# Kernel optimization log

Measured on AMD Instinct MI355X. Metric: run time of the kernel, lower is better.

## Reference

```python
import jax, jax.numpy as jnp
import numpy as np

OUT_DIM = 1024


def setup_inputs() -> dict:
    key = jax.random.key(0)
    k1, k2, k3, k4 = jax.random.split(key, 4)
    B, N, D = 4, 2048, 1024
    s = 1.0 / np.sqrt(D)
    return {
        "x": jax.random.normal(k1, (B, N, D), dtype=jnp.float32),
        "W_query": jax.random.normal(k2, (D, OUT_DIM), dtype=jnp.float32) * s,
        "W_key": jax.random.normal(k3, (D, OUT_DIM), dtype=jnp.float32) * s,
        "W_value": jax.random.normal(k4, (D, OUT_DIM), dtype=jnp.float32) * s,
    }


def reference(x, W_query, W_key, W_value):
    # x: [B, N, D_in]; W_*: [D_in, D_out] (torch Linear weight transposed)
    q = jnp.einsum("bnd,de->bne", x, W_query)
    k = jnp.einsum("bnd,de->bne", x, W_key)
    v = jnp.einsum("bnd,de->bne", x, W_value)
    sqrt_d = jnp.sqrt(jnp.asarray(OUT_DIM, dtype=jnp.float32))
    scores = jnp.einsum("bie,bje->bij", q, k) / sqrt_d  # [B, N, N]
    # NOTE: original uses softmax over dim=1 (query axis), not the usual dim=2
    attn = jax.nn.softmax(scores, axis=1)
    # dropout with train=False is identity (eval-mode reference)
    # out = attn^T @ v  ->  out[b, j] = sum_i attn[b, i, j] * v[b, i]
    return jnp.einsum("bij,bie->bje", attn, v)
```

## Files before the change

### kernel.cpp

```cpp
#include <hip/hip_runtime.h>
#include <math.h>


typedef __bf16 bf16x8 __attribute__((ext_vector_type(8)));
typedef float f32x4 __attribute__((ext_vector_type(4)));

static __device__ __forceinline__ unsigned short f2bf(float f) {
    unsigned u = __float_as_uint(f);
    u += 0x7fff + ((u >> 16) & 1);
    return (unsigned short)(u >> 16);
}

#define GLDS16(gptr, lptr)                                                            \
    __builtin_amdgcn_global_load_lds(                                                 \
        (const __attribute__((address_space(1))) void*)(gptr),                        \
        (__attribute__((address_space(3))) void*)(lptr), 16, 0, 0)

#define BARSYNC  __builtin_amdgcn_s_barrier()
#define WAITLGKM do { asm volatile("s_waitcnt lgkmcnt(0)" ::: "memory");    \
                      __builtin_amdgcn_sched_barrier(0); } while (0)

__device__ __forceinline__ void gemm256_core(
    const unsigned short* __restrict__ Ab,
    const unsigned short* __restrict__ Bb,
    const long ld, unsigned short* lds, f32x4 acc[8][4])
{
    const int tid  = threadIdx.x;
    const int w    = tid >> 6;
    const int lane = tid & 63;

    const int r  = lane >> 3;
    const int s  = lane & 7;
    const int cg = (s ^ r) * 8;

    const int fr    = lane & 15;
    const int quad  = lane >> 4;
    const int sw    = fr & 7;
    const int arow0 = (w >> 2) * 128;
    const int brow0 = (w & 3) * 64;

#define STG_A(t, mh, buf) do {                                              \
    const int rb_ = (w >> 2) * 128 + (mh) * 64 + (w & 3) * 16;              \
    const unsigned short* g_ = Ab + (long)(rb_ + r) * ld + (long)(t) * 64 + cg; \
    unsigned short* d_ = lds + (buf) * 16384 + rb_ * 64;                    \
    GLDS16(g_, d_); GLDS16(g_ + 8 * ld, d_ + 512); } while (0)
#define STG_B(t, nh, buf) do {                                              \
    const int rb_ = (w >> 1) * 64 + (nh) * 32 + (w & 1) * 16;               \
    const unsigned short* g_ = Bb + (long)(rb_ + r) * ld + (long)(t) * 64 + cg; \
    unsigned short* d_ = lds + 32768 + (buf) * 16384 + rb_ * 64;            \
    GLDS16(g_, d_); GLDS16(g_ + 8 * ld, d_ + 512); } while (0)

    bf16x8 af[4][2], bfA[2][2], bfB[2][2];
#define LOADA(buf, mh) do {                                                 \
    _Pragma("unroll") for (int ks_ = 0; ks_ < 2; ks_++)                     \
    _Pragma("unroll") for (int i_ = 0; i_ < 4; i_++)                        \
        af[i_][ks_] = *(const bf16x8*)&lds[(buf) * 16384 +                  \
            (arow0 + (mh) * 64 + i_ * 16 + fr) * 64 +                       \
            ((ks_ * 4 + quad) ^ sw) * 8]; } while (0)
#define LOADB(BF, buf, nh) do {                                             \
    _Pragma("unroll") for (int ks_ = 0; ks_ < 2; ks_++)                     \
    _Pragma("unroll") for (int j_ = 0; j_ < 2; j_++)                        \
        BF[j_][ks_] = *(const bf16x8*)&lds[32768 + (buf) * 16384 +          \
            (brow0 + (nh) * 32 + j_ * 16 + fr) * 64 +                       \
            ((ks_ * 4 + quad) ^ sw) * 8]; } while (0)

#define MFMA16(mh, nh, BF) do {                                             \
    __builtin_amdgcn_s_setprio(1);                                          \
    _Pragma("unroll") for (int ks_ = 0; ks_ < 2; ks_++)                     \
    _Pragma("unroll") for (int i_ = 0; i_ < 4; i_++)                        \
    _Pragma("unroll") for (int j_ = 0; j_ < 2; j_++)                        \
        acc[(mh) * 4 + i_][(nh) * 2 + j_] =                                 \
            __builtin_amdgcn_mfma_f32_16x16x32_bf16(                        \
                af[i_][ks_], BF[j_][ks_],                                   \
                acc[(mh) * 4 + i_][(nh) * 2 + j_], 0, 0, 0);                \
    __builtin_amdgcn_s_setprio(0); } while (0)

#pragma unroll
    for (int i = 0; i < 8; i++)
#pragma unroll
        for (int j = 0; j < 4; j++) acc[i][j] = f32x4{0.f, 0.f, 0.f, 0.f};

    STG_A(0, 0, 0); STG_A(0, 1, 0); STG_B(0, 0, 0); STG_B(0, 1, 0);
    STG_A(1, 0, 1); STG_B(1, 1, 1);
    asm volatile("s_waitcnt vmcnt(4)" ::: "memory");
    BARSYNC;

#pragma unroll 1
    for (int i = 0; i < 8; ++i) {
        const int t1 = 2 * i + 1;
        const int t2 = (2 * i + 2) & 15;
        const int t3 = (2 * i + 3) & 15;
        LOADA(0, 0); LOADB(bfA, 0, 0); STG_B(t1, 0, 1);
        BARSYNC; WAITLGKM; MFMA16(0, 0, bfA); BARSYNC;
        LOADB(bfB, 0, 1); STG_A(t1, 1, 1);
        BARSYNC; WAITLGKM; MFMA16(0, 1, bfB); BARSYNC;
        LOADA(0, 1); STG_A(t2, 0, 0);
        BARSYNC; WAITLGKM; MFMA16(1, 1, bfB); BARSYNC;
        STG_B(t2, 1, 0);
        BARSYNC; MFMA16(1, 0, bfA);
        asm volatile("s_waitcnt vmcnt(4)" ::: "memory"); BARSYNC;
        LOADA(1, 0); LOADB(bfA, 1, 0); STG_A(t2, 1, 0);
        BARSYNC; WAITLGKM; MFMA16(0, 0, bfA); BARSYNC;
        LOADB(bfB, 1, 1); STG_B(t2, 0, 0);
        BARSYNC; WAITLGKM; MFMA16(0, 1, bfB); BARSYNC;
        LOADA(1, 1); STG_A(t3, 0, 1);
        BARSYNC; WAITLGKM; MFMA16(1, 1, bfB); BARSYNC;
        STG_B(t3, 1, 1);
        BARSYNC; MFMA16(1, 0, bfA);
        asm volatile("s_waitcnt vmcnt(4)" ::: "memory"); BARSYNC;
    }
    asm volatile("s_waitcnt vmcnt(0)" ::: "memory");

#undef STG_A
#undef STG_B
#undef LOADA
#undef LOADB
#undef MFMA16
}

__device__ __forceinline__ void pv256_core(
    const unsigned short* __restrict__ Ab,
    const unsigned short* __restrict__ Bb,
    unsigned short* lds, f32x4 acc[8][2])
{
    const int tid  = threadIdx.x;
    const int w    = tid >> 6;
    const int lane = tid & 63;

    const int r  = lane >> 3;
    const int s  = lane & 7;
    const int cg = (s ^ r) * 8;

    const int fr    = lane & 15;
    const int quad  = lane >> 4;
    const int sw    = fr & 7;
    const int arow0 = (w >> 2) * 128;
    const int brow0 = (w & 3) * 32;

#define STG_PA(t, mh, buf) do {                                             \
    const int rb_ = (w >> 2) * 128 + (mh) * 64 + (w & 3) * 16;              \
    const unsigned short* g_ = Ab + (long)(rb_ + r) * 2048 + (long)(t) * 64 + cg; \
    unsigned short* d_ = lds + (buf) * 16384 + rb_ * 64;                    \
    GLDS16(g_, d_); GLDS16(g_ + 8 * 2048, d_ + 512); } while (0)
#define STG_PB(t, nh, buf) do {                                             \
    const int rb_ = (w & 3) * 32 + (nh) * 16 + (w >> 2) * 8;                \
    const unsigned short* g_ = Bb + (long)(rb_ + r) * 8192 + (long)(t) * 64 + cg; \
    unsigned short* d_ = lds + 32768 + (buf) * 8192 + rb_ * 64;             \
    GLDS16(g_, d_); } while (0)

    bf16x8 af[4][2], bfA[2], bfB[2];
#define LOADPA(buf, mh) do {                                                \
    _Pragma("unroll") for (int ks_ = 0; ks_ < 2; ks_++)                     \
    _Pragma("unroll") for (int i_ = 0; i_ < 4; i_++)                        \
        af[i_][ks_] = *(const bf16x8*)&lds[(buf) * 16384 +                  \
            (arow0 + (mh) * 64 + i_ * 16 + fr) * 64 +                       \
            ((ks_ * 4 + quad) ^ sw) * 8]; } while (0)
#define LOADPB(BF, buf, nh) do {                                            \
    _Pragma("unroll") for (int ks_ = 0; ks_ < 2; ks_++)                     \
        BF[ks_] = *(const bf16x8*)&lds[32768 + (buf) * 8192 +               \
            (brow0 + (nh) * 16 + fr) * 64 +                                 \
            ((ks_ * 4 + quad) ^ sw) * 8]; } while (0)

#define MFMA8(mh, nh, BF) do {                                              \
    __builtin_amdgcn_s_setprio(1);                                          \
    _Pragma("unroll") for (int ks_ = 0; ks_ < 2; ks_++)                     \
    _Pragma("unroll") for (int i_ = 0; i_ < 4; i_++)                        \
        acc[(mh) * 4 + i_][nh] = __builtin_amdgcn_mfma_f32_16x16x32_bf16(   \
            af[i_][ks_], BF[ks_], acc[(mh) * 4 + i_][nh], 0, 0, 0);         \
    __builtin_amdgcn_s_setprio(0); } while (0)

#pragma unroll
    for (int i = 0; i < 8; i++)
#pragma unroll
        for (int j = 0; j < 2; j++) acc[i][j] = f32x4{0.f, 0.f, 0.f, 0.f};

    STG_PA(0, 0, 0); STG_PA(0, 1, 0); STG_PB(0, 0, 0); STG_PB(0, 1, 0);
    STG_PA(1, 0, 1); STG_PB(1, 1, 1);
    asm volatile("s_waitcnt vmcnt(3)" ::: "memory");
    BARSYNC;

#pragma unroll 1
    for (int i = 0; i < 16; ++i) {
        const int t1 = 2 * i + 1;
        const int t2 = (2 * i + 2) & 31;
        const int t3 = (2 * i + 3) & 31;
        LOADPA(0, 0); LOADPB(bfA, 0, 0); STG_PB(t1, 0, 1);
        BARSYNC; WAITLGKM; MFMA8(0, 0, bfA); BARSYNC;
        LOADPB(bfB, 0, 1); STG_PA(t1, 1, 1);
        BARSYNC; WAITLGKM; MFMA8(0, 1, bfB); BARSYNC;
        LOADPA(0, 1); STG_PA(t2, 0, 0);
        BARSYNC; WAITLGKM; MFMA8(1, 1, bfB); BARSYNC;
        STG_PB(t2, 1, 0);
        BARSYNC; MFMA8(1, 0, bfA);
        asm volatile("s_waitcnt vmcnt(3)" ::: "memory"); BARSYNC;
        LOADPA(1, 0); LOADPB(bfA, 1, 0); STG_PA(t2, 1, 0);
        BARSYNC; WAITLGKM; MFMA8(0, 0, bfA); BARSYNC;
        LOADPB(bfB, 1, 1); STG_PB(t2, 0, 0);
        BARSYNC; WAITLGKM; MFMA8(0, 1, bfB); BARSYNC;
        LOADPA(1, 1); STG_PA(t3, 0, 1);
        BARSYNC; WAITLGKM; MFMA8(1, 1, bfB); BARSYNC;
        STG_PB(t3, 1, 1);
        BARSYNC; MFMA8(1, 0, bfA);
        asm volatile("s_waitcnt vmcnt(3)" ::: "memory"); BARSYNC;
    }
    asm volatile("s_waitcnt vmcnt(0)" ::: "memory");

#undef STG_PA
#undef STG_PB
#undef LOADPA
#undef LOADPB
#undef MFMA8
}

__global__ __launch_bounds__(512, 2) void gemm_qkv256(
    const unsigned short* __restrict__ A, const unsigned short* __restrict__ B,
    unsigned short* __restrict__ QK, unsigned short* __restrict__ Vt)
{
    __shared__ unsigned short lds[65536];
    const int orig = blockIdx.x;
    const int xcd  = orig & 7;
    const int pos  = orig >> 3;
    const long gm0 = (long)(xcd * 4 + (pos & 3)) * 256;
    const long gn0 = (long)(pos >> 2) * 256;

    f32x4 acc[8][4];
    gemm256_core(A + gm0 * 1024, B + gn0 * 1024, 1024, lds, acc);

    const int tid = threadIdx.x;
    const int w = tid >> 6, lane = tid & 63;
    const int fr = lane & 15, quad = lane >> 4;
    const int wm = (w >> 2) * 128, wn = (w & 3) * 64;

    if (gn0 < 2048) {
#pragma unroll
        for (int mi = 0; mi < 8; mi++) {
            const long rb = gm0 + wm + (mi >> 2) * 64 + (mi & 3) * 16 + quad * 4;
#pragma unroll
            for (int n = 0; n < 4; n++) {
                const long cb = gn0 + wn + n * 16 + fr;
#pragma unroll
                for (int rr = 0; rr < 4; rr++)
                    QK[(rb + rr) * 2048L + cb] = f2bf(acc[mi][n][rr]);
            }
        }
    } else {
#pragma unroll
        for (int mi = 0; mi < 8; mi++) {
            const long rb = gm0 + wm + (mi >> 2) * 64 + (mi & 3) * 16 + quad * 4;
#pragma unroll
            for (int n = 0; n < 4; n++) {
                const long ce = gn0 - 2048 + wn + n * 16 + fr;
                ushort4 o;
                o.x = f2bf(acc[mi][n][0]);
                o.y = f2bf(acc[mi][n][1]);
                o.z = f2bf(acc[mi][n][2]);
                o.w = f2bf(acc[mi][n][3]);
                *(ushort4*)&Vt[ce * 8192L + rb] = o;
            }
        }
    }
}

__global__ __launch_bounds__(512, 2) void gemm_scores256(
    const unsigned short* __restrict__ QKb, unsigned short* __restrict__ P,
    float* __restrict__ l)
{
    __shared__ unsigned short lds[65536];
    const int orig = blockIdx.x;
    const int xcd  = orig & 7;
    const int pos  = orig >> 3;
    const int bz   = xcd >> 1;
    const long gm0 = (long)((xcd & 1) * 4 + (pos >> 3)) * 256;
    const long gn0 = (long)(pos & 7) * 256;

    const unsigned short* Ab = QKb + (long)bz * 2048 * 2048 + 1024 + gm0 * 2048;
    const unsigned short* Bb = QKb + (long)bz * 2048 * 2048 + gn0 * 2048;

    f32x4 acc[8][4];
    gemm256_core(Ab, Bb, 2048, lds, acc);

    const int tid = threadIdx.x;
    const int w = tid >> 6, lane = tid & 63;
    const int fr = lane & 15, quad = lane >> 4;
    const int wm = (w >> 2) * 128, wn = (w & 3) * 64;

    unsigned short* Pb = P + (long)bz * 2048 * 2048;
    float* lb = l + (long)bz * 2048;
    const float scale = 1.0f / 32.0f;
#pragma unroll
    for (int mi = 0; mi < 8; mi++) {
        const long rb = gm0 + wm + (mi >> 2) * 64 + (mi & 3) * 16 + quad * 4;
        float rs[4] = {0.f, 0.f, 0.f, 0.f};
#pragma unroll
        for (int n = 0; n < 4; n++) {
            const long cb = gn0 + wn + n * 16 + fr;
#pragma unroll
            for (int rr = 0; rr < 4; rr++) {
                float e = __expf(acc[mi][n][rr] * scale);
                rs[rr] += e;
                Pb[(rb + rr) * 2048L + cb] = f2bf(e);
            }
        }
#pragma unroll
        for (int rr = 0; rr < 4; rr++) {
#pragma unroll
            for (int m = 8; m > 0; m >>= 1) rs[rr] += __shfl_xor(rs[rr], m, 16);
        }
        if (fr == 0) {
#pragma unroll
            for (int rr = 0; rr < 4; rr++)
                atomicAdd(&lb[rb + rr], rs[rr]);
        }
    }
}

__global__ __launch_bounds__(512, 2) void gemm_pv256(
    const unsigned short* __restrict__ P, const unsigned short* __restrict__ Vt,
    const float* __restrict__ l, float* __restrict__ out)
{
    __shared__ unsigned short lds[49152];
    const int orig = blockIdx.x;
    const int xcd  = orig & 7;
    const int pos  = orig >> 3;
    const int bz   = xcd >> 1;
    const long gm0 = (long)((xcd & 1) * 4 + (pos >> 3)) * 256;
    const long gn0 = (long)(pos & 7) * 128;

    const unsigned short* Ab = P + (long)bz * 2048 * 2048 + gm0 * 2048;
    const unsigned short* Bb = Vt + gn0 * 8192 + (long)bz * 2048;

    f32x4 acc[8][2];
    pv256_core(Ab, Bb, lds, acc);

    const int tid = threadIdx.x;
    const int w = tid >> 6, lane = tid & 63;
    const int fr = lane & 15, quad = lane >> 4;
    const int wm = (w >> 2) * 128, wn = (w & 3) * 32;

    float* Ob = out + (long)bz * 2048 * 1024;
    const float* lb = l + (long)bz * 2048;
#pragma unroll
    for (int mi = 0; mi < 8; mi++) {
        const long rb = gm0 + wm + (mi >> 2) * 64 + (mi & 3) * 16 + quad * 4;
        float inv[4];
#pragma unroll
        for (int rr = 0; rr < 4; rr++) inv[rr] = 1.0f / lb[rb + rr];
#pragma unroll
        for (int nj = 0; nj < 2; nj++) {
            const long cb = gn0 + wn + nj * 16 + fr;
#pragma unroll
            for (int rr = 0; rr < 4; rr++)
                Ob[(rb + rr) * 1024L + cb] = acc[mi][nj][rr] * inv[rr];
        }
    }
}

__global__ __launch_bounds__(256) void prep(
    const float* __restrict__ x,
    const float* __restrict__ Wq, const float* __restrict__ Wk,
    const float* __restrict__ Wv,
    unsigned short* __restrict__ xb, unsigned short* __restrict__ Wqkvt,
    float* __restrict__ l)
{
    __shared__ float t[32][33];
    const int b = blockIdx.x;
    const int tid = threadIdx.x;
    if (b < 8192) {
        int i = b * 256 + tid;
        float4 v = ((const float4*)x)[i];
        ushort4 o;
        o.x = f2bf(v.x); o.y = f2bf(v.y); o.z = f2bf(v.z); o.w = f2bf(v.w);
        ((ushort4*)xb)[i] = o;
        return;
    }
    if (b == 8192 + 3072) {
        float4 z = {0.f, 0.f, 0.f, 0.f};
#pragma unroll
        for (int i = 0; i < 8; i++)
            ((float4*)l)[tid * 8 + i] = z;
        return;
    }
    int tix = b - 8192;
    const int w = tix >> 10;
    tix &= 1023;
    const float* W = (w == 0) ? Wq : (w == 1) ? Wk : Wv;
    unsigned short* Wt = Wqkvt + (long)w * 1024 * 1024;
    const int bx = (tix & 31) * 32;
    const int by = (tix >> 5) * 32;
    const int tx = tid & 31;
    const int ty = (tid >> 5) * 4;
#pragma unroll
    for (int j = 0; j < 4; j++)
        t[ty + j][tx] = W[(long)(by + ty + j) * 1024 + bx + tx];
    __syncthreads();
#pragma unroll
    for (int j = 0; j < 4; j++)
        Wt[(long)(bx + ty + j) * 1024 + by + tx] = f2bf(t[tx][ty + j]);
}

extern "C" void kernel_launch(void* const* d_in, const int* in_sizes, int n_in,
                              void* d_out, int out_size, void* d_ws,
                              size_t ws_size, hipStream_t stream)
{
    const float* x  = (const float*)d_in[0];
    const float* Wq = (const float*)d_in[1];
    const float* Wk = (const float*)d_in[2];
    const float* Wv = (const float*)d_in[3];
    float* out = (float*)d_out;

    const long M1 = 1024 * 1024;
    unsigned short* u     = (unsigned short*)d_ws;
    unsigned short* xb    = u;
    unsigned short* Wqkvt = u + 8 * M1;
    unsigned short* QKb   = Wqkvt + 3 * M1;
    unsigned short* Vtb   = QKb + 16 * M1;
    unsigned short* Pb    = Vtb + 8 * M1;
    float* l              = (float*)(Pb + 16 * M1);

    prep<<<dim3(8192 + 3072 + 1), dim3(256), 0, stream>>>(x, Wq, Wk, Wv, xb, Wqkvt, l);

    gemm_qkv256<<<dim3(384), dim3(512), 0, stream>>>(xb, Wqkvt, QKb, Vtb);

    gemm_scores256<<<dim3(256), dim3(512), 0, stream>>>(QKb, Pb, l);

    gemm_pv256<<<dim3(256), dim3(512), 0, stream>>>(Pb, Vtb, l, out);
}
```

Measured before the change: 227.4 us.

## Split QKV GEMM into QK kernel and separate 128x256-tile V kernel

```diff
diff --git a/kernel.cpp b/kernel.cpp
--- a/kernel.cpp
+++ b/kernel.cpp
@@ -118,6 +118,104 @@
 #undef MFMA16
 }
 
+__device__ __forceinline__ void gemm_v128_core(
+    const unsigned short* __restrict__ Ab,
+    const unsigned short* __restrict__ Bb,
+    unsigned short* lds, f32x4 acc[4][4])
+{
+    const int tid  = threadIdx.x;
+    const int w    = tid >> 6;
+    const int lane = tid & 63;
+
+    const int r  = lane >> 3;
+    const int s  = lane & 7;
+    const int cg = (s ^ r) * 8;
+
+    const int fr    = lane & 15;
+    const int quad  = lane >> 4;
+    const int sw    = fr & 7;
+    const int arow0 = (w >> 2) * 64;
+    const int brow0 = (w & 3) * 64;
+
+#define STG_VA(t, mh, buf) do {                                             \
+    const int rb_ = (w >> 2) * 64 + (mh) * 32 + (w & 3) * 8;                \
+    const unsigned short* g_ = Ab + (long)(rb_ + r) * 1024 + (long)(t) * 64 + cg; \
+    unsigned short* d_ = lds + (buf) * 8192 + rb_ * 64;                     \
+    GLDS16(g_, d_); } while (0)
+#define STG_VB(t, nh, buf) do {                                             \
+    const int rb_ = (w >> 1) * 64 + (nh) * 32 + (w & 1) * 16;               \
+    const unsigned short* g_ = Bb + (long)(rb_ + r) * 1024 + (long)(t) * 64 + cg; \
+    unsigned short* d_ = lds + 16384 + (buf) * 16384 + rb_ * 64;            \
+    GLDS16(g_, d_); GLDS16(g_ + 8 * 1024, d_ + 512); } while (0)
+
+    bf16x8 af[2][2], bfA[2][2], bfB[2][2];
+#define LOADVA(buf, mh) do {                                                \
+    _Pragma("unroll") for (int ks_ = 0; ks_ < 2; ks_++)                     \
+    _Pragma("unroll") for (int i_ = 0; i_ < 2; i_++)                        \
+        af[i_][ks_] = *(const bf16x8*)&lds[(buf) * 8192 +                   \
+            (arow0 + (mh) * 32 + i_ * 16 + fr) * 64 +                       \
+            ((ks_ * 4 + quad) ^ sw) * 8]; } while (0)
+#define LOADVB(BF, buf, nh) do {                                            \
+    _Pragma("unroll") for (int ks_ = 0; ks_ < 2; ks_++)                     \
+    _Pragma("unroll") for (int j_ = 0; j_ < 2; j_++)                        \
+        BF[j_][ks_] = *(const bf16x8*)&lds[16384 + (buf) * 16384 +          \
+            (brow0 + (nh) * 32 + j_ * 16 + fr) * 64 +                       \
+            ((ks_ * 4 + quad) ^ sw) * 8]; } while (0)
+
+#define MFMA_V(mh, nh, BF) do {                                             \
+    __builtin_amdgcn_s_setprio(1);                                          \
+    _Pragma("unroll") for (int ks_ = 0; ks_ < 2; ks_++)                     \
+    _Pragma("unroll") for (int i_ = 0; i_ < 2; i_++)                        \
+    _Pragma("unroll") for (int j_ = 0; j_ < 2; j_++)                        \
+        acc[(mh) * 2 + i_][(nh) * 2 + j_] =                                 \
+            __builtin_amdgcn_mfma_f32_16x16x32_bf16(                        \
+                af[i_][ks_], BF[j_][ks_],                                   \
+                acc[(mh) * 2 + i_][(nh) * 2 + j_], 0, 0, 0);                \
+    __builtin_amdgcn_s_setprio(0); } while (0)
+
+#pragma unroll
+    for (int i = 0; i < 4; i++)
+#pragma unroll
+        for (int j = 0; j < 4; j++) acc[i][j] = f32x4{0.f, 0.f, 0.f, 0.f};
+
+    STG_VA(0, 0, 0); STG_VA(0, 1, 0); STG_VB(0, 0, 0); STG_VB(0, 1, 0);
+    STG_VA(1, 0, 1); STG_VB(1, 1, 1);
+    asm volatile("s_waitcnt vmcnt(3)" ::: "memory");
+    BARSYNC;
+
+#pragma unroll 1
+    for (int i = 0; i < 8; ++i) {
+        const int t1 = 2 * i + 1;
+        const int t2 = (2 * i + 2) & 15;
+        const int t3 = (2 * i + 3) & 15;
+        LOADVA(0, 0); LOADVB(bfA, 0, 0); STG_VB(t1, 0, 1);
+        BARSYNC; WAITLGKM; MFMA_V(0, 0, bfA); BARSYNC;
+        LOADVB(bfB, 0, 1); STG_VA(t1, 1, 1);
+        BARSYNC; WAITLGKM; MFMA_V(0, 1, bfB); BARSYNC;
+        LOADVA(0, 1); STG_VA(t2, 0, 0);
+        BARSYNC; WAITLGKM; MFMA_V(1, 1, bfB); BARSYNC;
+        STG_VB(t2, 1, 0);
+        BARSYNC; MFMA_V(1, 0, bfA);
+        asm volatile("s_waitcnt vmcnt(3)" ::: "memory"); BARSYNC;
+        LOADVA(1, 0); LOADVB(bfA, 1, 0); STG_VA(t2, 1, 0);
+        BARSYNC; WAITLGKM; MFMA_V(0, 0, bfA); BARSYNC;
+        LOADVB(bfB, 1, 1); STG_VB(t2, 0, 0);
+        BARSYNC; WAITLGKM; MFMA_V(0, 1, bfB); BARSYNC;
+        LOADVA(1, 1); STG_VA(t3, 0, 1);
+        BARSYNC; WAITLGKM; MFMA_V(1, 1, bfB); BARSYNC;
+        STG_VB(t3, 1, 1);
+        BARSYNC; MFMA_V(1, 0, bfA);
+        asm volatile("s_waitcnt vmcnt(3)" ::: "memory"); BARSYNC;
+    }
+    asm volatile("s_waitcnt vmcnt(0)" ::: "memory");
+
+#undef STG_VA
+#undef STG_VB
+#undef LOADVA
+#undef LOADVB
+#undef MFMA_V
+}
+
 __device__ __forceinline__ void pv256_core(
     const unsigned short* __restrict__ Ab,
     const unsigned short* __restrict__ Bb,
@@ -212,9 +310,9 @@
 #undef MFMA8
 }
 
-__global__ __launch_bounds__(512, 2) void gemm_qkv256(
+__global__ __launch_bounds__(512, 2) void gemm_qk256(
     const unsigned short* __restrict__ A, const unsigned short* __restrict__ B,
-    unsigned short* __restrict__ QK, unsigned short* __restrict__ Vt)
+    unsigned short* __restrict__ QK)
 {
     __shared__ unsigned short lds[65536];
     const int orig = blockIdx.x;
@@ -231,32 +329,50 @@
     const int fr = lane & 15, quad = lane >> 4;
     const int wm = (w >> 2) * 128, wn = (w & 3) * 64;
 
-    if (gn0 < 2048) {
-#pragma unroll
-        for (int mi = 0; mi < 8; mi++) {
-            const long rb = gm0 + wm + (mi >> 2) * 64 + (mi & 3) * 16 + quad * 4;
-#pragma unroll
-            for (int n = 0; n < 4; n++) {
-                const long cb = gn0 + wn + n * 16 + fr;
-#pragma unroll
-                for (int rr = 0; rr < 4; rr++)
-                    QK[(rb + rr) * 2048L + cb] = f2bf(acc[mi][n][rr]);
-            }
+#pragma unroll
+    for (int mi = 0; mi < 8; mi++) {
+        const long rb = gm0 + wm + (mi >> 2) * 64 + (mi & 3) * 16 + quad * 4;
+#pragma unroll
+        for (int n = 0; n < 4; n++) {
+            const long cb = gn0 + wn + n * 16 + fr;
+#pragma unroll
+            for (int rr = 0; rr < 4; rr++)
+                QK[(rb + rr) * 2048L + cb] = f2bf(acc[mi][n][rr]);
         }
-    } else {
-#pragma unroll
-        for (int mi = 0; mi < 8; mi++) {
-            const long rb = gm0 + wm + (mi >> 2) * 64 + (mi & 3) * 16 + quad * 4;
-#pragma unroll
-            for (int n = 0; n < 4; n++) {
-                const long ce = gn0 - 2048 + wn + n * 16 + fr;
-                ushort4 o;
-                o.x = f2bf(acc[mi][n][0]);
-                o.y = f2bf(acc[mi][n][1]);
-                o.z = f2bf(acc[mi][n][2]);
-                o.w = f2bf(acc[mi][n][3]);
-                *(ushort4*)&Vt[ce * 8192L + rb] = o;
-            }
+    }
+}
+
+__global__ __launch_bounds__(512, 2) void gemm_v128(
+    const unsigned short* __restrict__ A, const unsigned short* __restrict__ B,
+    unsigned short* __restrict__ Vt)
+{
+    __shared__ unsigned short lds[49152];
+    const int orig = blockIdx.x;
+    const int xcd  = orig & 7;
+    const int pos  = orig >> 3;
+    const long gm0 = (long)(xcd * 8 + (pos & 7)) * 128;
+    const long gn0 = (long)(pos >> 3) * 256;
+
+    f32x4 acc[4][4];
+    gemm_v128_core(A + gm0 * 1024, B + gn0 * 1024, lds, acc);
+
+    const int tid = threadIdx.x;
+    const int w = tid >> 6, lane = tid & 63;
+    const int fr = lane & 15, quad = lane >> 4;
+    const int wm = (w >> 2) * 64, wn = (w & 3) * 64;
+
+#pragma unroll
+    for (int ai = 0; ai < 4; ai++) {
+        const long rb = gm0 + wm + ai * 16 + quad * 4;
+#pragma unroll
+        for (int aj = 0; aj < 4; aj++) {
+            const long ce = gn0 + wn + aj * 16 + fr;
+            ushort4 o;
+            o.x = f2bf(acc[ai][aj][0]);
+            o.y = f2bf(acc[ai][aj][1]);
+            o.z = f2bf(acc[ai][aj][2]);
+            o.w = f2bf(acc[ai][aj][3]);
+            *(ushort4*)&Vt[ce * 8192L + rb] = o;
         }
     }
 }
@@ -419,7 +535,9 @@
 
     prep<<<dim3(8192 + 3072 + 1), dim3(256), 0, stream>>>(x, Wq, Wk, Wv, xb, Wqkvt, l);
 
-    gemm_qkv256<<<dim3(384), dim3(512), 0, stream>>>(xb, Wqkvt, QKb, Vtb);
+    gemm_qk256<<<dim3(256), dim3(512), 0, stream>>>(xb, Wqkvt, QKb);
+
+    gemm_v128<<<dim3(256), dim3(512), 0, stream>>>(xb, Wqkvt + 2 * M1, Vtb);
 
     gemm_scores256<<<dim3(256), dim3(512), 0, stream>>>(QKb, Pb, l);
 
```

After: 221.0 us. -2.8%, faster.
